# Performance work log

Measured on AMD Instinct MI355X. Metric: run time of the kernel, lower is better.

Reference implementation:

```python
import jax, jax.numpy as jnp
import numpy as np

N_NODES = 50000
N_EDGES = 800000
D = 128


def setup_inputs() -> dict:
    key = jax.random.key(0)
    ks = jax.random.split(key, 6)
    node_features = jax.random.normal(ks[0], (N_NODES, D), dtype=jnp.float32)
    edge_index = jax.random.randint(ks[1], (2, N_EDGES), 0, N_NODES, dtype=jnp.int64)
    s = 1.0 / np.sqrt(D)
    W1 = jax.random.normal(ks[2], (D, D), dtype=jnp.float32) * s
    b1 = jnp.zeros((D,), dtype=jnp.float32)
    W2 = jax.random.normal(ks[3], (D, D), dtype=jnp.float32) * s
    b2 = jnp.zeros((D,), dtype=jnp.float32)
    eta = jax.random.normal(ks[4], (1, 1), dtype=jnp.float32) * 0.5
    ln_gamma = jnp.ones((D,), dtype=jnp.float32)
    ln_beta = jnp.zeros((D,), dtype=jnp.float32)
    return {"node_features": node_features, "edge_index": edge_index,
            "W1": W1, "b1": b1, "W2": W2, "b2": b2, "eta": eta,
            "ln_gamma": ln_gamma, "ln_beta": ln_beta}


def _layer_norm(x, gamma, beta, eps=1e-5):
    mu = jnp.mean(x, axis=-1, keepdims=True)
    var = jnp.var(x, axis=-1, keepdims=True)
    return (x - mu) * jax.lax.rsqrt(var + eps) * gamma + beta


def reference(node_features, edge_index, W1, b1, W2, b2, eta, ln_gamma, ln_beta):
    initial = node_features
    src, dst = edge_index[0], edge_index[1]
    # gather neighbor features and sum-aggregate per destination node
    hu = node_features[src]                                   # [E, D]
    sum_hu = jax.ops.segment_sum(hu, dst, num_segments=node_features.shape[0])
    z = (1.0 + eta) * node_features + sum_hu                  # [N, D]
    # MLP: Linear -> ReLU -> Linear -> ReLU, then outer ReLU (idempotent)
    h = jax.nn.relu(z @ W1.T + b1)
    h = jax.nn.relu(h @ W2.T + b2)
    h = jax.nn.relu(h)
    h = _layer_norm(h, ln_gamma, ln_beta)                     # dropout p=0 -> identity
    return h + initial                                        # skip connection
```

## Files before the change

### kernel.cpp

```cpp
#include <hip/hip_runtime.h>

#define NN 50000
#define NE 800000
#define DD 128

typedef unsigned int u32;
typedef unsigned short u16;
typedef unsigned long long u64;
typedef __attribute__((ext_vector_type(8))) short bf16x8;
typedef __attribute__((ext_vector_type(4))) float f32x4;

__device__ __forceinline__ float bf2f(u16 u) {
    union { float f; u32 i; } v; v.i = ((u32)u) << 16; return v.f;
}
__device__ __forceinline__ u16 f2bf(float f) {
    u32 x = __float_as_uint(f);
    x += 0x7fffu + ((x >> 16) & 1u);
    return (u16)(x >> 16);
}

__global__ __launch_bounds__(64) void gin_detect(const u32* __restrict__ xw,
                                                 const u32* __restrict__ ew,
                                                 int* __restrict__ flags) {
    int lane = threadIdx.x;
    u32 w = xw[lane];
    u32 e8 = (w >> 7) & 0xFFu;
    bool bfOK = (e8 >= 100u && e8 <= 150u) || ((w & 0xFFFFu) == 0u);
    u64 m1 = __ballot(bfOK);
    bool oddZero = (ew[2 * lane + 1] == 0u);
    u64 m2 = __ballot(oddZero);
    if (lane == 0) {
        flags[0] = (__popcll(m1) >= 56) ? 1 : 0;
        flags[1] = (__popcll(m2) >= 60) ? 1 : 0;
    }
}

__global__ __launch_bounds__(256) void gin_tobf(const void* __restrict__ xv,
                                                uint4* __restrict__ xb,
                                                const int* __restrict__ flags) {
    int i = blockIdx.x * 256 + threadIdx.x;
    const int nu = NN * DD / 8;
    if (i >= nu) return;
    if (flags[0]) {
        xb[i] = ((const uint4*)xv)[i];
    } else {
        float4 a0 = ((const float4*)xv)[2 * i + 0];
        float4 a1 = ((const float4*)xv)[2 * i + 1];
        uint4 p;
        p.x = (u32)f2bf(a0.x) | ((u32)f2bf(a0.y) << 16);
        p.y = (u32)f2bf(a0.z) | ((u32)f2bf(a0.w) << 16);
        p.z = (u32)f2bf(a1.x) | ((u32)f2bf(a1.y) << 16);
        p.w = (u32)f2bf(a1.z) | ((u32)f2bf(a1.w) << 16);
        xb[i] = p;
    }
}

__global__ __launch_bounds__(256) void gin_zero(u32* __restrict__ deg) {
    int i = blockIdx.x * 256 + threadIdx.x;
    if (i < NN) deg[i] = 0u;
}

__global__ __launch_bounds__(256) void gin_hist(const int* __restrict__ ei,
                                                u32* __restrict__ deg,
                                                u16* __restrict__ rank,
                                                const int* __restrict__ flags) {
    int e = blockIdx.x * 256 + threadIdx.x;
    if (e >= NE) return;
    int d = flags[1] ? ei[2 * (NE + e)] : ei[NE + e];
    rank[e] = (u16)atomicAdd(&deg[d], 1u);
}

#define SCAN_CHUNK 2048
#define NSB ((NN + SCAN_CHUNK - 1) / SCAN_CHUNK)

__global__ __launch_bounds__(1024) void gin_scan1(const u32* __restrict__ deg,
                                                  u32* __restrict__ partials) {
    __shared__ u32 red[1024];
    int tid = threadIdx.x;
    int base = blockIdx.x * SCAN_CHUNK + tid * 2;
    u32 a = (base < NN) ? deg[base] : 0u;
    u32 b = (base + 1 < NN) ? deg[base + 1] : 0u;
    red[tid] = a + b;
    __syncthreads();
    for (int off = 512; off > 0; off >>= 1) {
        if (tid < off) red[tid] += red[tid + off];
        __syncthreads();
    }
    if (tid == 0) partials[blockIdx.x] = red[0];
}

__global__ __launch_bounds__(64) void gin_scan2(u32* __restrict__ partials) {
    int lane = threadIdx.x;
    u32 orig = (lane < NSB) ? partials[lane] : 0u;
    u32 v = orig;
    for (int off = 1; off < 64; off <<= 1) {
        u32 t = __shfl_up(v, off);
        if (lane >= off) v += t;
    }
    if (lane < NSB) partials[lane] = v - orig;
}

__global__ __launch_bounds__(1024) void gin_scan3(const u32* __restrict__ deg,
                                                  const u32* __restrict__ partials,
                                                  u32* __restrict__ row_start) {
    __shared__ u32 sc[1024];
    int tid = threadIdx.x;
    int base = blockIdx.x * SCAN_CHUNK + tid * 2;
    u32 a = (base < NN) ? deg[base] : 0u;
    u32 b = (base + 1 < NN) ? deg[base + 1] : 0u;
    u32 ts = a + b;
    sc[tid] = ts;
    __syncthreads();
    for (int off = 1; off < 1024; off <<= 1) {
        u32 v = (tid >= off) ? sc[tid - off] : 0u;
        __syncthreads();
        sc[tid] += v;
        __syncthreads();
    }
    u32 excl = sc[tid] - ts + partials[blockIdx.x];
    if (base < NN) row_start[base] = excl;
    if (base + 1 < NN) row_start[base + 1] = excl + a;
}

__global__ __launch_bounds__(256) void gin_fill(const int* __restrict__ ei,
                                                const u32* __restrict__ row_start,
                                                const u16* __restrict__ rank,
                                                u16* __restrict__ bs,
                                                const int* __restrict__ flags) {
    int e = blockIdx.x * 256 + threadIdx.x;
    if (e >= NE) return;
    int s, d;
    if (flags[1]) { s = ei[2 * e]; d = ei[2 * (NE + e)]; }
    else          { s = ei[e];     d = ei[NE + e]; }
    bs[row_start[d] + (u32)rank[e]] = (u16)s;
}

__global__ __launch_bounds__(256) void gin_gather(const u32* __restrict__ xb,
                                                  const u16* __restrict__ bs,
                                                  const u32* __restrict__ row_start,
                                                  const u32* __restrict__ deg,
                                                  const void* __restrict__ etav,
                                                  u32* __restrict__ zb,
                                                  const int* __restrict__ flags) {
    int node = blockIdx.x * 4 + (threadIdx.x >> 6);
    if (node >= NN) return;
    const int lane = threadIdx.x & 63;
    float s = 1.0f + (flags[0] ? bf2f(((const u16*)etav)[0]) : ((const float*)etav)[0]);
    u32 p = xb[(size_t)node * 64 + lane];
    float ax = bf2f((u16)(p & 0xffffu)) * s;
    float ay = bf2f((u16)(p >> 16)) * s;
    u32 jb = row_start[node], je = jb + deg[node];
    u32 j = jb;
    for (; j + 3 < je; j += 4) {
        u32 s0 = bs[j], s1 = bs[j + 1], s2 = bs[j + 2], s3 = bs[j + 3];
        u32 p0 = xb[(size_t)s0 * 64 + lane];
        u32 p1 = xb[(size_t)s1 * 64 + lane];
        u32 p2 = xb[(size_t)s2 * 64 + lane];
        u32 p3 = xb[(size_t)s3 * 64 + lane];
        ax += bf2f((u16)(p0 & 0xffffu)) + bf2f((u16)(p1 & 0xffffu))
            + bf2f((u16)(p2 & 0xffffu)) + bf2f((u16)(p3 & 0xffffu));
        ay += bf2f((u16)(p0 >> 16)) + bf2f((u16)(p1 >> 16))
            + bf2f((u16)(p2 >> 16)) + bf2f((u16)(p3 >> 16));
    }
    for (; j < je; ++j) {
        u32 p0 = xb[(size_t)bs[j] * 64 + lane];
        ax += bf2f((u16)(p0 & 0xffffu));
        ay += bf2f((u16)(p0 >> 16));
    }
    zb[(size_t)node * 64 + lane] = (u32)f2bf(ax) | ((u32)f2bf(ay) << 16);
}

__global__ __launch_bounds__(256) void gin_init(const void* __restrict__ xv,
                                                const void* __restrict__ etav,
                                                float* __restrict__ z,
                                                const int* __restrict__ flags) {
    int i = blockIdx.x * 256 + threadIdx.x;
    const int n8 = NN * DD / 8;
    if (i >= n8) return;
    const int fbf = flags[0];
    float s = 1.0f + (fbf ? bf2f(((const u16*)etav)[0]) : ((const float*)etav)[0]);
    float4 a, b;
    if (fbf) {
        uint4 p = ((const uint4*)xv)[i];
        a.x = bf2f((u16)(p.x & 0xffffu)); a.y = bf2f((u16)(p.x >> 16));
        a.z = bf2f((u16)(p.y & 0xffffu)); a.w = bf2f((u16)(p.y >> 16));
        b.x = bf2f((u16)(p.z & 0xffffu)); b.y = bf2f((u16)(p.z >> 16));
        b.z = bf2f((u16)(p.w & 0xffffu)); b.w = bf2f((u16)(p.w >> 16));
    } else {
        a = ((const float4*)xv)[2 * i + 0];
        b = ((const float4*)xv)[2 * i + 1];
    }
    a.x *= s; a.y *= s; a.z *= s; a.w *= s;
    b.x *= s; b.y *= s; b.z *= s; b.w *= s;
    ((float4*)z)[2 * i + 0] = a;
    ((float4*)z)[2 * i + 1] = b;
}

__global__ __launch_bounds__(256) void gin_scatter(const void* __restrict__ xv,
                                                   const int* __restrict__ ei,
                                                   float* __restrict__ z,
                                                   const int* __restrict__ flags) {
    int e = blockIdx.x * 4 + (threadIdx.x >> 6);
    if (e >= NE) return;
    const int fbf = flags[0];
    const int f64 = flags[1];
    int lane = threadIdx.x & 63;
    int s, d;
    if (f64) { s = ei[2 * e]; d = ei[2 * (NE + e)]; }
    else     { s = ei[e];     d = ei[NE + e]; }
    float v0, v1;
    if (fbf) {
        u32 p = ((const u32*)((const u16*)xv + (size_t)s * DD))[lane];
        v0 = bf2f((u16)(p & 0xffffu));
        v1 = bf2f((u16)(p >> 16));
    } else {
        float2 p = ((const float2*)((const float*)xv + (size_t)s * DD))[lane];
        v0 = p.x; v1 = p.y;
    }
    float* dst = z + (size_t)d * DD + 2 * lane;
    atomicAdd(dst + 0, v0);
    atomicAdd(dst + 1, v1);
}

#define TRM 64
#define NTM ((NN + TRM - 1) / TRM)

template <int FBF, int ZBF>
__global__ __launch_bounds__(512, 1) void gin_mlp(
    const void* __restrict__ zv, const void* __restrict__ xskip,
    const void* __restrict__ W1, const void* __restrict__ b1,
    const void* __restrict__ W2, const void* __restrict__ b2,
    const void* __restrict__ gamma, const void* __restrict__ beta,
    float* __restrict__ out, const int* __restrict__ flags) {
    if (flags[0] != FBF) return;

    __shared__ short s_w1[DD * DD];
    __shared__ short s_w2[DD * DD];
    __shared__ short s_zt[TRM * DD];
    __shared__ short s_h1[TRM * DD];
    __shared__ float s_h2[TRM * 132];

    const int tid = threadIdx.x;
    char* w1c = (char*)s_w1;
    char* w2c = (char*)s_w2;
    char* ztc = (char*)s_zt;
    char* h1c = (char*)s_h1;

    if (FBF) {
#pragma unroll
        for (int q = 0; q < 4; ++q) {
            int u = tid + q * 512;
            int row = u >> 4, cu = u & 15;
            uint4 a = ((const uint4*)W1)[u];
            uint4 c = ((const uint4*)W2)[u];
            int off = row * 256 + ((cu ^ (row & 7)) << 4);
            *(uint4*)(w1c + off) = a;
            *(uint4*)(w2c + off) = c;
        }
    } else {
#pragma unroll
        for (int q = 0; q < 4; ++q) {
            int u = tid + q * 512;
            int row = u >> 4, cu = u & 15;
            float4 a0 = ((const float4*)W1)[u * 2 + 0];
            float4 a1 = ((const float4*)W1)[u * 2 + 1];
            float4 c0 = ((const float4*)W2)[u * 2 + 0];
            float4 c1 = ((const float4*)W2)[u * 2 + 1];
            uint4 pa, pc;
            pa.x = (u32)f2bf(a0.x) | ((u32)f2bf(a0.y) << 16);
            pa.y = (u32)f2bf(a0.z) | ((u32)f2bf(a0.w) << 16);
            pa.z = (u32)f2bf(a1.x) | ((u32)f2bf(a1.y) << 16);
            pa.w = (u32)f2bf(a1.z) | ((u32)f2bf(a1.w) << 16);
            pc.x = (u32)f2bf(c0.x) | ((u32)f2bf(c0.y) << 16);
            pc.y = (u32)f2bf(c0.z) | ((u32)f2bf(c0.w) << 16);
            pc.z = (u32)f2bf(c1.x) | ((u32)f2bf(c1.y) << 16);
            pc.w = (u32)f2bf(c1.z) | ((u32)f2bf(c1.w) << 16);
            int off = row * 256 + ((cu ^ (row & 7)) << 4);
            *(uint4*)(w1c + off) = pa;
            *(uint4*)(w2c + off) = pc;
        }
    }

    const int lane = tid & 63;
    const int wid = tid >> 6;
    const int lrow = lane & 15;
    const int hi = lane >> 4;
    const int rstrip = wid & 3;
    const int nb = (wid >> 2) * 64;
    const int arow = rstrip * 16 + lrow;

    float b1v[4], b2v[4];
#pragma unroll
    for (int tt = 0; tt < 4; ++tt) {
        int j = nb + tt * 16 + lrow;
        b1v[tt] = FBF ? bf2f(((const u16*)b1)[j]) : ((const float*)b1)[j];
        b2v[tt] = FBF ? bf2f(((const u16*)b2)[j]) : ((const float*)b2)[j];
    }

    const int cg = tid & 31;
    const int rg = tid >> 5;
    const int r0 = rg * 4;
    float gv[4], bev[4];
    if (FBF) {
        uint2 pg = ((const uint2*)gamma)[cg];
        uint2 pe = ((const uint2*)beta)[cg];
        gv[0] = bf2f((u16)(pg.x & 0xffffu)); gv[1] = bf2f((u16)(pg.x >> 16));
        gv[2] = bf2f((u16)(pg.y & 0xffffu)); gv[3] = bf2f((u16)(pg.y >> 16));
        bev[0] = bf2f((u16)(pe.x & 0xffffu)); bev[1] = bf2f((u16)(pe.x >> 16));
        bev[2] = bf2f((u16)(pe.y & 0xffffu)); bev[3] = bf2f((u16)(pe.y >> 16));
    } else {
        float4 t3 = ((const float4*)gamma)[cg];
        float4 t4 = ((const float4*)beta)[cg];
        gv[0] = t3.x; gv[1] = t3.y; gv[2] = t3.z; gv[3] = t3.w;
        bev[0] = t4.x; bev[1] = t4.y; bev[2] = t4.z; bev[3] = t4.w;
    }

    for (int t = blockIdx.x; t < NTM; t += gridDim.x) {
        const int row0 = t * TRM;
        __syncthreads();
        if (ZBF) {
#pragma unroll
            for (int q = 0; q < 2; ++q) {
                int u = tid + q * 512;
                int row = u >> 4, cu = u & 15;
                int grow = row0 + row;
                uint4 p = {0u, 0u, 0u, 0u};
                if (grow < NN) p = ((const uint4*)zv)[(size_t)grow * 16 + cu];
                *(uint4*)(ztc + row * 256 + ((cu ^ (row & 7)) << 4)) = p;
            }
        } else {
#pragma unroll
            for (int q = 0; q < 2; ++q) {
                int u = tid + q * 512;
                int row = u >> 4, cu = u & 15;
                int grow = row0 + row;
                float4 a0 = {0.f, 0.f, 0.f, 0.f}, a1 = {0.f, 0.f, 0.f, 0.f};
                if (grow < NN) {
                    a0 = ((const float4*)zv)[(size_t)grow * 32 + cu * 2 + 0];
                    a1 = ((const float4*)zv)[(size_t)grow * 32 + cu * 2 + 1];
                }
                uint4 p;
                p.x = (u32)f2bf(a0.x) | ((u32)f2bf(a0.y) << 16);
                p.y = (u32)f2bf(a0.z) | ((u32)f2bf(a0.w) << 16);
                p.z = (u32)f2bf(a1.x) | ((u32)f2bf(a1.y) << 16);
                p.w = (u32)f2bf(a1.z) | ((u32)f2bf(a1.w) << 16);
                *(uint4*)(ztc + row * 256 + ((cu ^ (row & 7)) << 4)) = p;
            }
        }
        __syncthreads();

        f32x4 acc[4];
#pragma unroll
        for (int tt = 0; tt < 4; ++tt)
            acc[tt] = (f32x4){b1v[tt], b1v[tt], b1v[tt], b1v[tt]};
#pragma unroll
        for (int c = 0; c < 4; ++c) {
            bf16x8 af = *(const bf16x8*)(ztc + arow * 256 + (((c * 4 + hi) ^ (arow & 7)) << 4));
#pragma unroll
            for (int tt = 0; tt < 4; ++tt) {
                int brow = nb + tt * 16 + lrow;
                bf16x8 bfv = *(const bf16x8*)(w1c + brow * 256 + (((c * 4 + hi) ^ (brow & 7)) << 4));
                acc[tt] = __builtin_amdgcn_mfma_f32_16x16x32_bf16(af, bfv, acc[tt], 0, 0, 0);
            }
        }
#pragma unroll
        for (int tt = 0; tt < 4; ++tt) {
            int j = nb + tt * 16 + lrow;
            int jb2 = j * 2;
            int unit = jb2 >> 4, within = jb2 & 15;
#pragma unroll
            for (int qq = 0; qq < 4; ++qq) {
                int row = rstrip * 16 + hi * 4 + qq;
                u16 hb = f2bf(fmaxf(acc[tt][qq], 0.f));
                *(u16*)(h1c + row * 256 + ((unit ^ (row & 7)) << 4) + within) = hb;
            }
        }
        __syncthreads();
#pragma unroll
        for (int tt = 0; tt < 4; ++tt)
            acc[tt] = (f32x4){b2v[tt], b2v[tt], b2v[tt], b2v[tt]};
#pragma unroll
        for (int c = 0; c < 4; ++c) {
            bf16x8 af = *(const bf16x8*)(h1c + arow * 256 + (((c * 4 + hi) ^ (arow & 7)) << 4));
#pragma unroll
            for (int tt = 0; tt < 4; ++tt) {
                int brow = nb + tt * 16 + lrow;
                bf16x8 bfv = *(const bf16x8*)(w2c + brow * 256 + (((c * 4 + hi) ^ (brow & 7)) << 4));
                acc[tt] = __builtin_amdgcn_mfma_f32_16x16x32_bf16(af, bfv, acc[tt], 0, 0, 0);
            }
        }
#pragma unroll
        for (int tt = 0; tt < 4; ++tt) {
            int j = nb + tt * 16 + lrow;
#pragma unroll
            for (int qq = 0; qq < 4; ++qq) {
                int row = rstrip * 16 + hi * 4 + qq;
                s_h2[row * 132 + j] = fmaxf(acc[tt][qq], 0.f);
            }
        }
        __syncthreads();
#pragma unroll
        for (int r = 0; r < 4; ++r) {
            const float* hp = &s_h2[(r0 + r) * 132 + 4 * cg];
            float h0 = hp[0], h1 = hp[1], h2 = hp[2], h3 = hp[3];
            float s1 = h0 + h1 + h2 + h3;
            float s2 = h0 * h0 + h1 * h1 + h2 * h2 + h3 * h3;
#pragma unroll
            for (int m = 1; m <= 16; m <<= 1) {
                s1 += __shfl_xor(s1, m);
                s2 += __shfl_xor(s2, m);
            }
            float mean = s1 * (1.0f / DD);
            float var = s2 * (1.0f / DD) - mean * mean;
            float rs = rsqrtf(var + 1e-5f);
            int grow = row0 + r0 + r;
            if (grow < NN) {
                float xi[4];
                if (FBF || ZBF) {
                    uint2 px = ((const uint2*)((const u16*)xskip + (size_t)grow * DD))[cg];
                    xi[0] = bf2f((u16)(px.x & 0xffffu)); xi[1] = bf2f((u16)(px.x >> 16));
                    xi[2] = bf2f((u16)(px.y & 0xffffu)); xi[3] = bf2f((u16)(px.y >> 16));
                } else {
                    float4 px = ((const float4*)((const float*)xskip + (size_t)grow * DD))[cg];
                    xi[0] = px.x; xi[1] = px.y; xi[2] = px.z; xi[3] = px.w;
                }
                float4 o;
                o.x = (h0 - mean) * rs * gv[0] + bev[0] + xi[0];
                o.y = (h1 - mean) * rs * gv[1] + bev[1] + xi[1];
                o.z = (h2 - mean) * rs * gv[2] + bev[2] + xi[2];
                o.w = (h3 - mean) * rs * gv[3] + bev[3] + xi[3];
                ((float4*)(out + (size_t)grow * DD))[cg] = o;
            }
        }
    }
}

extern "C" void kernel_launch(void* const* d_in, const int* in_sizes, int n_in,
                              void* d_out, int out_size, void* d_ws, size_t ws_size,
                              hipStream_t stream) {
    const void* x = d_in[0];
    const int* ei = (const int*)d_in[1];
    const void* W1 = d_in[2];
    const void* b1 = d_in[3];
    const void* W2 = d_in[4];
    const void* b2 = d_in[5];
    const void* eta = d_in[6];
    const void* gamma = d_in[7];
    const void* beta = d_in[8];
    float* out = (float*)d_out;

    const size_t FLAGS_OFF = 0;
    const size_t PART_OFF = 64;
    const size_t Z_OFF = 256;
    const size_t ZB = (size_t)NN * DD * sizeof(float);
    const size_t XB_OFF = Z_OFF;
    const size_t ZBF_OFF = Z_OFF + (size_t)NN * DD * 2;
    const size_t DEG_OFF = Z_OFF + ZB;
    const size_t DEGB = 200192;
    const size_t RS_OFF = DEG_OFF + DEGB;
    const size_t RSB = 200448;
    const size_t BS_OFF = RS_OFF + RSB;
    const size_t BSB = (size_t)NE * sizeof(u16);
    const size_t RK_OFF = BS_OFF + BSB;
    const size_t RKB = (size_t)NE * sizeof(u16);
    const size_t TOT = RK_OFF + RKB;

    if (ws_size < Z_OFF + ZB) return;
    int* flags = (int*)((char*)d_ws + FLAGS_OFF);
    u32* partials = (u32*)((char*)d_ws + PART_OFF);

    gin_detect<<<1, 64, 0, stream>>>((const u32*)x, (const u32*)ei, flags);

    if (ws_size >= TOT) {
        u32* xb = (u32*)((char*)d_ws + XB_OFF);
        u32* zb = (u32*)((char*)d_ws + ZBF_OFF);
        u32* deg = (u32*)((char*)d_ws + DEG_OFF);
        u32* row_start = (u32*)((char*)d_ws + RS_OFF);
        u16* bs = (u16*)((char*)d_ws + BS_OFF);
        u16* rank = (u16*)((char*)d_ws + RK_OFF);
        gin_tobf<<<(NN * DD / 8 + 255) / 256, 256, 0, stream>>>(x, (uint4*)xb, flags);
        gin_zero<<<(NN + 255) / 256, 256, 0, stream>>>(deg);
        gin_hist<<<(NE + 255) / 256, 256, 0, stream>>>(ei, deg, rank, flags);
        gin_scan1<<<NSB, 1024, 0, stream>>>(deg, partials);
        gin_scan2<<<1, 64, 0, stream>>>(partials);
        gin_scan3<<<NSB, 1024, 0, stream>>>(deg, partials, row_start);
        gin_fill<<<(NE + 255) / 256, 256, 0, stream>>>(ei, row_start, rank, bs, flags);
        gin_gather<<<(NN + 3) / 4, 256, 0, stream>>>(xb, bs, row_start, deg, eta, zb, flags);
        gin_mlp<0, 1><<<256, 512, 0, stream>>>(zb, xb, W1, b1, W2, b2, gamma, beta, out, flags);
        gin_mlp<1, 1><<<256, 512, 0, stream>>>(zb, xb, W1, b1, W2, b2, gamma, beta, out, flags);
    } else {
        float* z = (float*)((char*)d_ws + Z_OFF);
        gin_init<<<(NN * DD / 8 + 255) / 256, 256, 0, stream>>>(x, eta, z, flags);
        gin_scatter<<<NE / 4, 256, 0, stream>>>(x, ei, z, flags);
        gin_mlp<0, 0><<<256, 512, 0, stream>>>(z, x, W1, b1, W2, b2, gamma, beta, out, flags);
        gin_mlp<1, 0><<<256, 512, 0, stream>>>(z, x, W1, b1, W2, b2, gamma, beta, out, flags);
    }
}
```

Before: 136.7 us.

## Merge tobf/zero kernels, fold scan2 into scan3, pack edges, unroll gather by 8

Fuses the bf16 conversion and degree-zeroing kernels into one launch. Drops the separate partials-scan kernel: each scan3 block now sums the preceding partials itself with a wave reduction. The histogram pass writes packed 16-bit src/dst pairs so the fill pass reads 4 bytes per edge instead of re-reading the int64 edge index. The gather loop is unrolled to 8 neighbours to keep more loads in flight. Together these cut launch count and memory traffic, at the cost of an extra 3.2MB workspace buffer. The packing assumes node ids fit in 16 bits, which does not hold for 50000 nodes shifted into the high half (fine, as d<65536).

After: 128.0 us. -6.4%, faster.

```diff
diff --git a/kernel.cpp b/kernel.cpp
--- a/kernel.cpp
+++ b/kernel.cpp
@@ -35,38 +35,46 @@
     }
 }
 
-__global__ __launch_bounds__(256) void gin_tobf(const void* __restrict__ xv,
-                                                uint4* __restrict__ xb,
-                                                const int* __restrict__ flags) {
-    int i = blockIdx.x * 256 + threadIdx.x;
-    const int nu = NN * DD / 8;
-    if (i >= nu) return;
-    if (flags[0]) {
-        xb[i] = ((const uint4*)xv)[i];
+#define NB_TOBF ((NN * DD / 8) / 256)
+#define NB_ZERO ((NN + 255) / 256)
+
+__global__ __launch_bounds__(256) void gin_tobf_zero(const void* __restrict__ xv,
+                                                     uint4* __restrict__ xb,
+                                                     u32* __restrict__ deg,
+                                                     const int* __restrict__ flags) {
+    int b = blockIdx.x;
+    int tid = threadIdx.x;
+    if (b < NB_TOBF) {
+        int i = b * 256 + tid;
+        if (flags[0]) {
+            xb[i] = ((const uint4*)xv)[i];
+        } else {
+            float4 a0 = ((const float4*)xv)[2 * i + 0];
+            float4 a1 = ((const float4*)xv)[2 * i + 1];
+            uint4 p;
+            p.x = (u32)f2bf(a0.x) | ((u32)f2bf(a0.y) << 16);
+            p.y = (u32)f2bf(a0.z) | ((u32)f2bf(a0.w) << 16);
+            p.z = (u32)f2bf(a1.x) | ((u32)f2bf(a1.y) << 16);
+            p.w = (u32)f2bf(a1.z) | ((u32)f2bf(a1.w) << 16);
+            xb[i] = p;
+        }
     } else {
-        float4 a0 = ((const float4*)xv)[2 * i + 0];
-        float4 a1 = ((const float4*)xv)[2 * i + 1];
-        uint4 p;
-        p.x = (u32)f2bf(a0.x) | ((u32)f2bf(a0.y) << 16);
-        p.y = (u32)f2bf(a0.z) | ((u32)f2bf(a0.w) << 16);
-        p.z = (u32)f2bf(a1.x) | ((u32)f2bf(a1.y) << 16);
-        p.w = (u32)f2bf(a1.z) | ((u32)f2bf(a1.w) << 16);
-        xb[i] = p;
-    }
-}
-
-__global__ __launch_bounds__(256) void gin_zero(u32* __restrict__ deg) {
-    int i = blockIdx.x * 256 + threadIdx.x;
-    if (i < NN) deg[i] = 0u;
+        int i = (b - NB_TOBF) * 256 + tid;
+        if (i < NN) deg[i] = 0u;
+    }
 }
 
 __global__ __launch_bounds__(256) void gin_hist(const int* __restrict__ ei,
                                                 u32* __restrict__ deg,
                                                 u16* __restrict__ rank,
+                                                u32* __restrict__ pck,
                                                 const int* __restrict__ flags) {
     int e = blockIdx.x * 256 + threadIdx.x;
     if (e >= NE) return;
-    int d = flags[1] ? ei[2 * (NE + e)] : ei[NE + e];
+    int s, d;
+    if (flags[1]) { s = ei[2 * e]; d = ei[2 * (NE + e)]; }
+    else          { s = ei[e];     d = ei[NE + e]; }
+    pck[e] = (u32)s | ((u32)d << 16);
     rank[e] = (u16)atomicAdd(&deg[d], 1u);
 }
 
@@ -89,22 +97,18 @@
     if (tid == 0) partials[blockIdx.x] = red[0];
 }
 
-__global__ __launch_bounds__(64) void gin_scan2(u32* __restrict__ partials) {
-    int lane = threadIdx.x;
-    u32 orig = (lane < NSB) ? partials[lane] : 0u;
-    u32 v = orig;
-    for (int off = 1; off < 64; off <<= 1) {
-        u32 t = __shfl_up(v, off);
-        if (lane >= off) v += t;
-    }
-    if (lane < NSB) partials[lane] = v - orig;
-}
-
 __global__ __launch_bounds__(1024) void gin_scan3(const u32* __restrict__ deg,
                                                   const u32* __restrict__ partials,
                                                   u32* __restrict__ row_start) {
     __shared__ u32 sc[1024];
+    __shared__ u32 chunk_base;
     int tid = threadIdx.x;
+    if (tid < 64) {
+        u32 v = (tid < NSB && tid < blockIdx.x) ? partials[tid] : 0u;
+#pragma unroll
+        for (int m = 32; m > 0; m >>= 1) v += __shfl_xor(v, m);
+        if (tid == 0) chunk_base = v;
+    }
     int base = blockIdx.x * SCAN_CHUNK + tid * 2;
     u32 a = (base < NN) ? deg[base] : 0u;
     u32 b = (base + 1 < NN) ? deg[base + 1] : 0u;
@@ -117,21 +121,19 @@
         sc[tid] += v;
         __syncthreads();
     }
-    u32 excl = sc[tid] - ts + partials[blockIdx.x];
+    u32 excl = sc[tid] - ts + chunk_base;
     if (base < NN) row_start[base] = excl;
     if (base + 1 < NN) row_start[base + 1] = excl + a;
 }
 
-__global__ __launch_bounds__(256) void gin_fill(const int* __restrict__ ei,
+__global__ __launch_bounds__(256) void gin_fill(const u32* __restrict__ pck,
                                                 const u32* __restrict__ row_start,
                                                 const u16* __restrict__ rank,
-                                                u16* __restrict__ bs,
-                                                const int* __restrict__ flags) {
+                                                u16* __restrict__ bs) {
     int e = blockIdx.x * 256 + threadIdx.x;
     if (e >= NE) return;
-    int s, d;
-    if (flags[1]) { s = ei[2 * e]; d = ei[2 * (NE + e)]; }
-    else          { s = ei[e];     d = ei[NE + e]; }
+    u32 p = pck[e];
+    u32 s = p & 0xffffu, d = p >> 16;
     bs[row_start[d] + (u32)rank[e]] = (u16)s;
 }
 
@@ -151,12 +153,32 @@
     float ay = bf2f((u16)(p >> 16)) * s;
     u32 jb = row_start[node], je = jb + deg[node];
     u32 j = jb;
+    for (; j + 7 < je; j += 8) {
+        u32 i0 = bs[j], i1 = bs[j + 1], i2 = bs[j + 2], i3 = bs[j + 3];
+        u32 i4 = bs[j + 4], i5 = bs[j + 5], i6 = bs[j + 6], i7 = bs[j + 7];
+        u32 p0 = xb[(size_t)i0 * 64 + lane];
+        u32 p1 = xb[(size_t)i1 * 64 + lane];
+        u32 p2 = xb[(size_t)i2 * 64 + lane];
+        u32 p3 = xb[(size_t)i3 * 64 + lane];
+        u32 p4 = xb[(size_t)i4 * 64 + lane];
+        u32 p5 = xb[(size_t)i5 * 64 + lane];
+        u32 p6 = xb[(size_t)i6 * 64 + lane];
+        u32 p7 = xb[(size_t)i7 * 64 + lane];
+        ax += bf2f((u16)(p0 & 0xffffu)) + bf2f((u16)(p1 & 0xffffu))
+            + bf2f((u16)(p2 & 0xffffu)) + bf2f((u16)(p3 & 0xffffu))
+            + bf2f((u16)(p4 & 0xffffu)) + bf2f((u16)(p5 & 0xffffu))
+            + bf2f((u16)(p6 & 0xffffu)) + bf2f((u16)(p7 & 0xffffu));
+        ay += bf2f((u16)(p0 >> 16)) + bf2f((u16)(p1 >> 16))
+            + bf2f((u16)(p2 >> 16)) + bf2f((u16)(p3 >> 16))
+            + bf2f((u16)(p4 >> 16)) + bf2f((u16)(p5 >> 16))
+            + bf2f((u16)(p6 >> 16)) + bf2f((u16)(p7 >> 16));
+    }
     for (; j + 3 < je; j += 4) {
-        u32 s0 = bs[j], s1 = bs[j + 1], s2 = bs[j + 2], s3 = bs[j + 3];
-        u32 p0 = xb[(size_t)s0 * 64 + lane];
-        u32 p1 = xb[(size_t)s1 * 64 + lane];
-        u32 p2 = xb[(size_t)s2 * 64 + lane];
-        u32 p3 = xb[(size_t)s3 * 64 + lane];
+        u32 i0 = bs[j], i1 = bs[j + 1], i2 = bs[j + 2], i3 = bs[j + 3];
+        u32 p0 = xb[(size_t)i0 * 64 + lane];
+        u32 p1 = xb[(size_t)i1 * 64 + lane];
+        u32 p2 = xb[(size_t)i2 * 64 + lane];
+        u32 p3 = xb[(size_t)i3 * 64 + lane];
         ax += bf2f((u16)(p0 & 0xffffu)) + bf2f((u16)(p1 & 0xffffu))
             + bf2f((u16)(p2 & 0xffffu)) + bf2f((u16)(p3 & 0xffffu));
         ay += bf2f((u16)(p0 >> 16)) + bf2f((u16)(p1 >> 16))
@@ -463,7 +485,9 @@
     const size_t BSB = (size_t)NE * sizeof(u16);
     const size_t RK_OFF = BS_OFF + BSB;
     const size_t RKB = (size_t)NE * sizeof(u16);
-    const size_t TOT = RK_OFF + RKB;
+    const size_t PCK_OFF = RK_OFF + RKB;
+    const size_t PCKB = (size_t)NE * sizeof(u32);
+    const size_t TOT = PCK_OFF + PCKB;
 
     if (ws_size < Z_OFF + ZB) return;
     int* flags = (int*)((char*)d_ws + FLAGS_OFF);
@@ -478,13 +502,12 @@
         u32* row_start = (u32*)((char*)d_ws + RS_OFF);
         u16* bs = (u16*)((char*)d_ws + BS_OFF);
         u16* rank = (u16*)((char*)d_ws + RK_OFF);
-        gin_tobf<<<(NN * DD / 8 + 255) / 256, 256, 0, stream>>>(x, (uint4*)xb, flags);
-        gin_zero<<<(NN + 255) / 256, 256, 0, stream>>>(deg);
-        gin_hist<<<(NE + 255) / 256, 256, 0, stream>>>(ei, deg, rank, flags);
+        u32* pck = (u32*)((char*)d_ws + PCK_OFF);
+        gin_tobf_zero<<<NB_TOBF + NB_ZERO, 256, 0, stream>>>(x, (uint4*)xb, deg, flags);
+        gin_hist<<<(NE + 255) / 256, 256, 0, stream>>>(ei, deg, rank, pck, flags);
         gin_scan1<<<NSB, 1024, 0, stream>>>(deg, partials);
-        gin_scan2<<<1, 64, 0, stream>>>(partials);
         gin_scan3<<<NSB, 1024, 0, stream>>>(deg, partials, row_start);
-        gin_fill<<<(NE + 255) / 256, 256, 0, stream>>>(ei, row_start, rank, bs, flags);
+        gin_fill<<<(NE + 255) / 256, 256, 0, stream>>>(pck, row_start, rank, bs);
         gin_gather<<<(NN + 3) / 4, 256, 0, stream>>>(xb, bs, row_start, deg, eta, zb, flags);
         gin_mlp<0, 1><<<256, 512, 0, stream>>>(zb, xb, W1, b1, W2, b2, gamma, beta, out, flags);
         gin_mlp<1, 1><<<256, 512, 0, stream>>>(zb, xb, W1, b1, W2, b2, gamma, beta, out, flags);
```
